# Kernel tuning notes

Hardware: AMD Instinct MI355X
Metric: run time of the kernel (lower is better)

## Reference

```python
import jax, jax.numpy as jnp
import numpy as np

HIDDEN = 1024
HEADS = 16
HEAD_DIM = HIDDEN // HEADS


def setup_inputs() -> dict:
    key = jax.random.key(0)
    ks = jax.random.split(key, 12)
    B, S, D = 2, 2048, HIDDEN
    scale = 1.0 / np.sqrt(D)
    return {
        "query": jax.random.normal(ks[0], (B, S, D), jnp.float32),
        "key": jax.random.normal(ks[1], (B, S, D), jnp.float32),
        "value": jax.random.normal(ks[2], (B, S, D), jnp.float32),
        "Wq": jax.random.normal(ks[3], (D, D), jnp.float32) * scale,
        "bq": jnp.zeros((D,), jnp.float32),
        "Wk": jax.random.normal(ks[4], (D, D), jnp.float32) * scale,
        "bk": jnp.zeros((D,), jnp.float32),
        "Wv": jax.random.normal(ks[5], (D, D), jnp.float32) * scale,
        "bv": jnp.zeros((D,), jnp.float32),
        "Wo": jax.random.normal(ks[6], (D, D), jnp.float32) * scale,
        "bo": jnp.zeros((D,), jnp.float32),
    }


def reference(query, key, value, Wq, bq, Wk, bk, Wv, bv, Wo, bo):
    B, S, D = query.shape
    H, Hd = HEADS, HEAD_DIM
    sm_scale = 1.0 / jnp.sqrt(jnp.asarray(Hd, query.dtype))

    def proj(x, W, b):  # nn.Linear: x @ W.T + b, then split heads -> [B,H,S,Hd]
        y = jnp.einsum("bsd,ed->bse", x, W) + b
        return y.reshape(B, S, H, Hd).transpose(0, 2, 1, 3)

    Q = proj(query, Wq, bq)
    K = proj(key, Wk, bk)
    V = proj(value, Wv, bv)

    scores = jnp.einsum("bhqd,bhkd->bhqk", Q, K) * sm_scale  # [B,H,S,S]
    attn = jax.nn.softmax(scores, axis=-1)
    ctx = jnp.einsum("bhqk,bhkd->bhqd", attn, V)
    ctx = ctx.transpose(0, 2, 1, 3).reshape(B, S, D)
    out = jnp.einsum("bsd,ed->bse", ctx, Wo) + bo
    return out
```

## Files before the change

kernel.cpp:

```cpp
#include <hip/hip_runtime.h>
#include <stdint.h>

typedef unsigned short u16;
typedef unsigned int u32;
typedef __attribute__((ext_vector_type(8))) short s16x8;
typedef __attribute__((ext_vector_type(4))) float fx4;

#define AS_GLOBAL __attribute__((address_space(1)))
#define AS_LDS    __attribute__((address_space(3)))

__device__ __forceinline__ void g2l16(const u16* g, u16* l) {
  __builtin_amdgcn_global_load_lds((const AS_GLOBAL unsigned int*)g,
                                   (AS_LDS unsigned int*)l, 16, 0, 0);
}
__device__ __forceinline__ u16 f2bf(float f) {
  u32 u = __float_as_uint(f);
  u += 0x7FFF + ((u >> 16) & 1);
  return (u16)(u >> 16);
}
__device__ __forceinline__ u32 pk2bf(float a, float b) {
  return (u32)f2bf(a) | ((u32)f2bf(b) << 16);
}

__global__ __launch_bounds__(256) void cvt3(const float* __restrict__ a, const float* __restrict__ b,
                                            const float* __restrict__ c, u16* oa, u16* ob, u16* oc, int n4) {
  const float* src = blockIdx.y == 0 ? a : blockIdx.y == 1 ? b : c;
  u16* dst = blockIdx.y == 0 ? oa : blockIdx.y == 1 ? ob : oc;
  int i = blockIdx.x * 256 + threadIdx.x;
  if (i >= n4) return;
  float4 f = ((const float4*)src)[i];
  ushort4 o; o.x = f2bf(f.x); o.y = f2bf(f.y); o.z = f2bf(f.z); o.w = f2bf(f.w);
  ((ushort4*)dst)[i] = o;
}
__global__ __launch_bounds__(256) void cvt4(const float* __restrict__ a, const float* __restrict__ b,
                                            const float* __restrict__ c, const float* __restrict__ d,
                                            u16* oa, u16* ob, u16* oc, u16* od, int n4) {
  const float* src = blockIdx.y == 0 ? a : blockIdx.y == 1 ? b : blockIdx.y == 2 ? c : d;
  u16* dst = blockIdx.y == 0 ? oa : blockIdx.y == 1 ? ob : blockIdx.y == 2 ? oc : od;
  int i = blockIdx.x * 256 + threadIdx.x;
  if (i >= n4) return;
  float4 f = ((const float4*)src)[i];
  ushort4 o; o.x = f2bf(f.x); o.y = f2bf(f.y); o.z = f2bf(f.z); o.w = f2bf(f.w);
  ((ushort4*)dst)[i] = o;
}

__global__ __launch_bounds__(256) void gemm_qkv(
    const u16* __restrict__ Aq, const u16* __restrict__ Ak, const u16* __restrict__ Av,
    const u16* __restrict__ Wq, const u16* __restrict__ Wk, const u16* __restrict__ Wv,
    const float* __restrict__ bq, const float* __restrict__ bk, const float* __restrict__ bv,
    u16* __restrict__ Oq, u16* __restrict__ Ok, u16* __restrict__ Ov)
{
  constexpr int K = 1024;
  __shared__ u16 As[128 * 32];
  __shared__ u16 Bs[128 * 32];
  const int z = blockIdx.z;
  const u16* A = z == 0 ? Aq : z == 1 ? Ak : Av;
  const u16* W = z == 0 ? Wq : z == 1 ? Wk : Wv;
  const float* bias = z == 0 ? bq : z == 1 ? bk : bv;
  u16* outB = z == 0 ? Oq : z == 1 ? Ok : Ov;
  const float scale = z == 0 ? 0.180336880f : 1.0f;

  const int bm = blockIdx.x, bn = blockIdx.y;
  const int tid = threadIdx.x;
  const int lane = tid & 63, wave = tid >> 6;
  const int quad = lane >> 4, col = lane & 15;
  const int wm = wave >> 1, wn = wave & 1;

  const int L0 = tid, L1 = 256 + tid;
  const int r0 = L0 >> 2, c0 = (L0 & 3) ^ ((r0 >> 1) & 3);
  const int r1 = L1 >> 2, c1 = (L1 & 3) ^ ((r1 >> 1) & 3);
  const u16* gA0 = A + (bm * 128 + r0) * K + c0 * 8;
  const u16* gA1 = A + (bm * 128 + r1) * K + c1 * 8;
  const u16* gB0 = W + (bn * 128 + r0) * K + c0 * 8;
  const u16* gB1 = W + (bn * 128 + r1) * K + c1 * 8;
  u16* lA0 = As + L0 * 8; u16* lA1 = As + L1 * 8;
  u16* lB0 = Bs + L0 * 8; u16* lB1 = Bs + L1 * 8;

  const int aRow = wm * 64 + col;
  const int bRow = wn * 64 + col;

  fx4 zero = {0.f, 0.f, 0.f, 0.f};
  fx4 acc[4][4];
#pragma unroll
  for (int i = 0; i < 4; ++i)
#pragma unroll
    for (int j = 0; j < 4; ++j) acc[i][j] = zero;

  for (int kb = 0; kb < K / 32; ++kb) {
    __syncthreads();
    g2l16(gA0 + kb * 32, lA0);
    g2l16(gA1 + kb * 32, lA1);
    g2l16(gB0 + kb * 32, lB0);
    g2l16(gB1 + kb * 32, lB1);
    __syncthreads();
    s16x8 af[4], bf[4];
#pragma unroll
    for (int mt = 0; mt < 4; ++mt) {
      int row = aRow + mt * 16;
      int ch = row * 4 + (quad ^ ((row >> 1) & 3));
      af[mt] = *(const s16x8*)(As + ch * 8);
    }
#pragma unroll
    for (int nt = 0; nt < 4; ++nt) {
      int row = bRow + nt * 16;
      int ch = row * 4 + (quad ^ ((row >> 1) & 3));
      bf[nt] = *(const s16x8*)(Bs + ch * 8);
    }
#pragma unroll
    for (int mt = 0; mt < 4; ++mt)
#pragma unroll
      for (int nt = 0; nt < 4; ++nt)
        acc[mt][nt] = __builtin_amdgcn_mfma_f32_16x16x32_bf16(af[mt], bf[nt], acc[mt][nt], 0, 0, 0);
  }

#pragma unroll
  for (int nt = 0; nt < 4; ++nt) {
    int n = bn * 128 + wn * 64 + nt * 16 + col;
    float bvv = bias[n];
#pragma unroll
    for (int mt = 0; mt < 4; ++mt) {
      int mbase = bm * 128 + wm * 64 + mt * 16 + quad * 4;
#pragma unroll
      for (int reg = 0; reg < 4; ++reg) {
        int m = mbase + reg;
        float v = (acc[mt][nt][reg] + bvv) * scale;
        int b = m >> 11, s = m & 2047;
        int h = n >> 6, hd = n & 63;
        outB[((b * 16 + h) * 2048 + s) * 64 + hd] = f2bf(v);
      }
    }
  }
}

__global__ __launch_bounds__(256) void gemm_out(
    const u16* __restrict__ A, const u16* __restrict__ W,
    const float* __restrict__ bias, float* __restrict__ outF)
{
  constexpr int K = 1024;
  __shared__ u16 As[128 * 32];
  __shared__ u16 Bs[64 * 32];
  const int bm = blockIdx.x, bn = blockIdx.y;
  const int tid = threadIdx.x;
  const int lane = tid & 63, wave = tid >> 6;
  const int quad = lane >> 4, col = lane & 15;
  const int wm = wave >> 1, wn = wave & 1;

  const int L0 = tid, L1 = 256 + tid;
  const int r0 = L0 >> 2, c0 = (L0 & 3) ^ ((r0 >> 1) & 3);
  const int r1 = L1 >> 2, c1 = (L1 & 3) ^ ((r1 >> 1) & 3);
  const u16* gA0 = A + (bm * 128 + r0) * K + c0 * 8;
  const u16* gA1 = A + (bm * 128 + r1) * K + c1 * 8;
  const u16* gB0 = W + (bn * 64 + r0) * K + c0 * 8;
  u16* lA0 = As + L0 * 8; u16* lA1 = As + L1 * 8;
  u16* lB0 = Bs + L0 * 8;

  const int aRow = wm * 64 + col;
  const int bRow = wn * 32 + col;

  fx4 zero = {0.f, 0.f, 0.f, 0.f};
  fx4 acc[4][2];
#pragma unroll
  for (int i = 0; i < 4; ++i)
#pragma unroll
    for (int j = 0; j < 2; ++j) acc[i][j] = zero;

  for (int kb = 0; kb < K / 32; ++kb) {
    __syncthreads();
    g2l16(gA0 + kb * 32, lA0);
    g2l16(gA1 + kb * 32, lA1);
    g2l16(gB0 + kb * 32, lB0);
    __syncthreads();
    s16x8 af[4], bf[2];
#pragma unroll
    for (int mt = 0; mt < 4; ++mt) {
      int row = aRow + mt * 16;
      int ch = row * 4 + (quad ^ ((row >> 1) & 3));
      af[mt] = *(const s16x8*)(As + ch * 8);
    }
#pragma unroll
    for (int nt = 0; nt < 2; ++nt) {
      int row = bRow + nt * 16;
      int ch = row * 4 + (quad ^ ((row >> 1) & 3));
      bf[nt] = *(const s16x8*)(Bs + ch * 8);
    }
#pragma unroll
    for (int mt = 0; mt < 4; ++mt)
#pragma unroll
      for (int nt = 0; nt < 2; ++nt)
        acc[mt][nt] = __builtin_amdgcn_mfma_f32_16x16x32_bf16(af[mt], bf[nt], acc[mt][nt], 0, 0, 0);
  }

#pragma unroll
  for (int nt = 0; nt < 2; ++nt) {
    int n = bn * 64 + wn * 32 + nt * 16 + col;
    float bvv = bias[n];
#pragma unroll
    for (int mt = 0; mt < 4; ++mt) {
      int mbase = bm * 128 + wm * 64 + mt * 16 + quad * 4;
#pragma unroll
      for (int reg = 0; reg < 4; ++reg)
        outF[(mbase + reg) * 1024 + n] = acc[mt][nt][reg] + bvv;
    }
  }
}

__global__ __launch_bounds__(256) void transpose_v(const u16* __restrict__ V,
                                                   u16* __restrict__ Vt) {
  __shared__ u16 tile[64 * 72];
  const int bh = blockIdx.y, s0 = blockIdx.x * 64;
  const int tid = threadIdx.x;
#pragma unroll
  for (int i = 0; i < 2; ++i) {
    int idx = i * 256 + tid;
    int s = idx >> 3, c = idx & 7;
    uint4 v = *(const uint4*)(V + ((size_t)bh * 2048 + s0 + s) * 64 + c * 8);
    const u16* pv = (const u16*)&v;
#pragma unroll
    for (int j = 0; j < 8; ++j) tile[(c * 8 + j) * 72 + s] = pv[j];
  }
  __syncthreads();
#pragma unroll
  for (int i = 0; i < 2; ++i) {
    int idx = i * 256 + tid;
    int d = idx >> 3, c = idx & 7;
    uint4 v = *(const uint4*)(tile + d * 72 + c * 8);
    *(uint4*)(Vt + ((size_t)bh * 64 + d) * 2048 + s0 + c * 8) = v;
  }
}

__global__ __launch_bounds__(256, 4) void flash_attn(
    const u16* __restrict__ Qp, const u16* __restrict__ Kp,
    const u16* __restrict__ Vt, u16* __restrict__ ctx)
{
  __shared__ u16 sh[16384];
  const int qt = blockIdx.x, bh = blockIdx.y;
  const int tid = threadIdx.x, lane = tid & 63, wave = tid >> 6;
  const int quad = lane >> 4, col = lane & 15;
  const int wm = wave >> 1, wn = wave & 1;

  const u16* Qb = Qp + ((size_t)bh * 2048 + qt * 64) * 64;
  const u16* Kb = Kp + (size_t)bh * 2048 * 64;
  const u16* Vb = Vt + (size_t)bh * 64 * 2048;

  s16x8 qf[2][2];
#pragma unroll
  for (int mt = 0; mt < 2; ++mt)
#pragma unroll
    for (int h = 0; h < 2; ++h)
      qf[mt][h] = *(const s16x8*)(Qb + (wm * 32 + mt * 16 + col) * 64 + h * 32 + quad * 8);

  fx4 zero = {0.f, 0.f, 0.f, 0.f};
  fx4 acc_o[2][4], acc_l[2];
#pragma unroll
  for (int mt = 0; mt < 2; ++mt) {
    acc_l[mt] = zero;
#pragma unroll
    for (int dt = 0; dt < 4; ++dt) acc_o[mt][dt] = zero;
  }
  s16x8 ones;
#pragma unroll
  for (int j = 0; j < 8; ++j) ones[j] = (short)0x3F80;

  u16* Vs = sh;
  u16* Pw = sh + 8192 + wave * 2048;

  for (int kv = 0; kv < 16; ++kv) {
    const int n0 = kv * 128;
    __syncthreads();
#pragma unroll
    for (int i = 0; i < 4; ++i) {
      int idx = wave * 256 + i * 64 + lane;
      int d = idx >> 4, c = idx & 15;
      uint4 v = *(const uint4*)(Vb + d * 2048 + n0 + c * 8);
      *(uint4*)(Vs + d * 128 + (c ^ (d & 15)) * 8) = v;
    }
#pragma unroll
    for (int nt = 0; nt < 4; ++nt) {
      const u16* kr = Kb + (n0 + wn * 64 + nt * 16 + col) * 64 + quad * 8;
      s16x8 k0 = *(const s16x8*)(kr);
      s16x8 k1 = *(const s16x8*)(kr + 32);
#pragma unroll
      for (int mt = 0; mt < 2; ++mt) {
        fx4 s = __builtin_amdgcn_mfma_f32_16x16x32_bf16(k0, qf[mt][0], zero, 0, 0, 0);
        s = __builtin_amdgcn_mfma_f32_16x16x32_bf16(k1, qf[mt][1], s, 0, 0, 0);
        int m = mt * 16 + col;
        int cch = 2 * nt + (quad >> 1);
        uint2 w;
        w.x = pk2bf(exp2f(s[0]), exp2f(s[1]));
        w.y = pk2bf(exp2f(s[2]), exp2f(s[3]));
        *(uint2*)(Pw + m * 64 + ((cch ^ (m & 7))) * 8 + (quad & 1) * 4) = w;
      }
    }
    __syncthreads();
#pragma unroll
    for (int ks = 0; ks < 2; ++ks) {
      s16x8 pf[2];
#pragma unroll
      for (int mt = 0; mt < 2; ++mt)
        pf[mt] = *(const s16x8*)(Pw + (mt * 16 + col) * 64 + ((4 * ks + quad) ^ (col & 7)) * 8);
#pragma unroll
      for (int dt = 0; dt < 4; ++dt) {
        s16x8 vf = *(const s16x8*)(Vs + (dt * 16 + col) * 128 + ((wn * 8 + 4 * ks + quad) ^ col) * 8);
#pragma unroll
        for (int mt = 0; mt < 2; ++mt)
          acc_o[mt][dt] = __builtin_amdgcn_mfma_f32_16x16x32_bf16(pf[mt], vf, acc_o[mt][dt], 0, 0, 0);
      }
#pragma unroll
      for (int mt = 0; mt < 2; ++mt)
        acc_l[mt] = __builtin_amdgcn_mfma_f32_16x16x32_bf16(pf[mt], ones, acc_l[mt], 0, 0, 0);
    }
  }

  __syncthreads();
  float* buf = (float*)sh;
  if (wn == 1) {
#pragma unroll
    for (int mt = 0; mt < 2; ++mt) {
#pragma unroll
      for (int dt = 0; dt < 4; ++dt)
#pragma unroll
        for (int e = 0; e < 4; ++e)
          buf[wm * 2560 + ((mt * 4 + dt) * 4 + e) * 64 + lane] = acc_o[mt][dt][e];
#pragma unroll
      for (int e = 0; e < 4; ++e)
        buf[wm * 2560 + (32 + mt * 4 + e) * 64 + lane] = acc_l[mt][e];
    }
  }
  __syncthreads();
  if (wn == 0) {
    const int b = bh >> 4, h = bh & 15;
#pragma unroll
    for (int mt = 0; mt < 2; ++mt) {
      fx4 rl;
#pragma unroll
      for (int e = 0; e < 4; ++e) {
        float l = acc_l[mt][e] + buf[wm * 2560 + (32 + mt * 4 + e) * 64 + lane];
        rl[e] = 1.0f / l;
      }
#pragma unroll
      for (int dt = 0; dt < 4; ++dt)
#pragma unroll
        for (int e = 0; e < 4; ++e) {
          float v = (acc_o[mt][dt][e] + buf[wm * 2560 + ((mt * 4 + dt) * 4 + e) * 64 + lane]) * rl[e];
          int s = qt * 64 + wm * 32 + mt * 16 + quad * 4 + e;
          ctx[((size_t)(b * 2048 + s)) * 1024 + h * 64 + dt * 16 + col] = f2bf(v);
        }
    }
  }
}

extern "C" void kernel_launch(void* const* d_in, const int* in_sizes, int n_in,
                              void* d_out, int out_size, void* d_ws, size_t ws_size,
                              hipStream_t stream) {
  const float* q  = (const float*)d_in[0];
  const float* k  = (const float*)d_in[1];
  const float* v  = (const float*)d_in[2];
  const float* Wq = (const float*)d_in[3];
  const float* bq = (const float*)d_in[4];
  const float* Wk = (const float*)d_in[5];
  const float* bk = (const float*)d_in[6];
  const float* Wv = (const float*)d_in[7];
  const float* bv = (const float*)d_in[8];
  const float* Wo = (const float*)d_in[9];
  const float* bo = (const float*)d_in[10];
  float* out = (float*)d_out;

  char* ws = (char*)d_ws;
  const size_t MB = 1u << 20;
  u16* qb  = (u16*)(ws + 0 * MB);
  u16* kb  = (u16*)(ws + 8 * MB);
  u16* vb  = (u16*)(ws + 16 * MB);
  u16* wqb = (u16*)(ws + 24 * MB);
  u16* wkb = (u16*)(ws + 26 * MB);
  u16* wvb = (u16*)(ws + 28 * MB);
  u16* wob = (u16*)(ws + 30 * MB);
  u16* Qp  = (u16*)(ws + 32 * MB);
  u16* Kp  = (u16*)(ws + 40 * MB);
  u16* Vp  = (u16*)(ws + 48 * MB);
  u16* Vtp = (u16*)(ws + 56 * MB);
  u16* ctx = (u16*)(ws + 64 * MB);

  cvt3<<<dim3(4096, 3), 256, 0, stream>>>(q, k, v, qb, kb, vb, 1048576);
  cvt4<<<dim3(1024, 4), 256, 0, stream>>>(Wq, Wk, Wv, Wo, wqb, wkb, wvb, wob, 262144);

  gemm_qkv<<<dim3(32, 8, 3), 256, 0, stream>>>(qb, kb, vb, wqb, wkb, wvb,
                                               bq, bk, bv, Qp, Kp, Vp);
  transpose_v<<<dim3(32, 32), 256, 0, stream>>>(Vp, Vtp);
  flash_attn<<<dim3(32, 32), 256, 0, stream>>>(Qp, Kp, Vtp, ctx);
  gemm_out<<<dim3(32, 16), 256, 0, stream>>>(ctx, wob, bo, out);
}
```

Baseline: 259.7 us.

## Fuse V transpose into QKV epilogue and keep P in registers for attention

The QKV GEMM epilogue now writes V directly in transposed [bh, d, s] layout, which removes the separate transpose kernel and its round trip through global memory. The flash-attention kernel no longer stages V and P through LDS. The probabilities stay in registers and feed 16x16x16 MFMAs, with V fragments loaded straight from global memory, which drops the two per-iteration block syncs. The two conversion kernels are merged into one launch. The tradeoffs are uncached, narrower V loads from global memory in the inner loop, twice as many MFMA instructions at half depth, and a removed occupancy hint.

```diff
diff --git a/kernel.cpp b/kernel.cpp
--- a/kernel.cpp
+++ b/kernel.cpp
@@ -4,6 +4,7 @@
 typedef unsigned short u16;
 typedef unsigned int u32;
 typedef __attribute__((ext_vector_type(8))) short s16x8;
+typedef __attribute__((ext_vector_type(4))) short s16x4;
 typedef __attribute__((ext_vector_type(4))) float fx4;
 
 #define AS_GLOBAL __attribute__((address_space(1)))
@@ -22,33 +23,34 @@
   return (u32)f2bf(a) | ((u32)f2bf(b) << 16);
 }
 
-__global__ __launch_bounds__(256) void cvt3(const float* __restrict__ a, const float* __restrict__ b,
-                                            const float* __restrict__ c, u16* oa, u16* ob, u16* oc, int n4) {
-  const float* src = blockIdx.y == 0 ? a : blockIdx.y == 1 ? b : c;
-  u16* dst = blockIdx.y == 0 ? oa : blockIdx.y == 1 ? ob : oc;
+__global__ __launch_bounds__(256) void cvt_all(
+    const float* __restrict__ q, const float* __restrict__ k, const float* __restrict__ v,
+    const float* __restrict__ wq, const float* __restrict__ wk, const float* __restrict__ wv,
+    const float* __restrict__ wo,
+    u16* oq, u16* ok, u16* ov, u16* owq, u16* owk, u16* owv, u16* owo) {
+  const int y = blockIdx.y;
+  const float* src; u16* dst; int n4;
+  switch (y) {
+    case 0: src = q;  dst = oq;  n4 = 1048576; break;
+    case 1: src = k;  dst = ok;  n4 = 1048576; break;
+    case 2: src = v;  dst = ov;  n4 = 1048576; break;
+    case 3: src = wq; dst = owq; n4 = 262144; break;
+    case 4: src = wk; dst = owk; n4 = 262144; break;
+    case 5: src = wv; dst = owv; n4 = 262144; break;
+    default: src = wo; dst = owo; n4 = 262144; break;
+  }
   int i = blockIdx.x * 256 + threadIdx.x;
   if (i >= n4) return;
   float4 f = ((const float4*)src)[i];
   ushort4 o; o.x = f2bf(f.x); o.y = f2bf(f.y); o.z = f2bf(f.z); o.w = f2bf(f.w);
   ((ushort4*)dst)[i] = o;
 }
-__global__ __launch_bounds__(256) void cvt4(const float* __restrict__ a, const float* __restrict__ b,
-                                            const float* __restrict__ c, const float* __restrict__ d,
-                                            u16* oa, u16* ob, u16* oc, u16* od, int n4) {
-  const float* src = blockIdx.y == 0 ? a : blockIdx.y == 1 ? b : blockIdx.y == 2 ? c : d;
-  u16* dst = blockIdx.y == 0 ? oa : blockIdx.y == 1 ? ob : blockIdx.y == 2 ? oc : od;
-  int i = blockIdx.x * 256 + threadIdx.x;
-  if (i >= n4) return;
-  float4 f = ((const float4*)src)[i];
-  ushort4 o; o.x = f2bf(f.x); o.y = f2bf(f.y); o.z = f2bf(f.z); o.w = f2bf(f.w);
-  ((ushort4*)dst)[i] = o;
-}
 
 __global__ __launch_bounds__(256) void gemm_qkv(
     const u16* __restrict__ Aq, const u16* __restrict__ Ak, const u16* __restrict__ Av,
     const u16* __restrict__ Wq, const u16* __restrict__ Wk, const u16* __restrict__ Wv,
     const float* __restrict__ bq, const float* __restrict__ bk, const float* __restrict__ bv,
-    u16* __restrict__ Oq, u16* __restrict__ Ok, u16* __restrict__ Ov)
+    u16* __restrict__ Oq, u16* __restrict__ Ok, u16* __restrict__ OvT)
 {
   constexpr int K = 1024;
   __shared__ u16 As[128 * 32];
@@ -57,7 +59,6 @@
   const u16* A = z == 0 ? Aq : z == 1 ? Ak : Av;
   const u16* W = z == 0 ? Wq : z == 1 ? Wk : Wv;
   const float* bias = z == 0 ? bq : z == 1 ? bk : bv;
-  u16* outB = z == 0 ? Oq : z == 1 ? Ok : Ov;
   const float scale = z == 0 ? 0.180336880f : 1.0f;
 
   const int bm = blockIdx.x, bn = blockIdx.y;
@@ -116,17 +117,22 @@
 #pragma unroll
   for (int nt = 0; nt < 4; ++nt) {
     int n = bn * 128 + wn * 64 + nt * 16 + col;
+    int h = n >> 6, hd = n & 63;
     float bvv = bias[n];
 #pragma unroll
     for (int mt = 0; mt < 4; ++mt) {
       int mbase = bm * 128 + wm * 64 + mt * 16 + quad * 4;
-#pragma unroll
-      for (int reg = 0; reg < 4; ++reg) {
-        int m = mbase + reg;
-        float v = (acc[mt][nt][reg] + bvv) * scale;
-        int b = m >> 11, s = m & 2047;
-        int h = n >> 6, hd = n & 63;
-        outB[((b * 16 + h) * 2048 + s) * 64 + hd] = f2bf(v);
+      int b = mbase >> 11, s = mbase & 2047;
+      if (z == 2) {
+        uint2 w;
+        w.x = pk2bf(acc[mt][nt][0] + bvv, acc[mt][nt][1] + bvv);
+        w.y = pk2bf(acc[mt][nt][2] + bvv, acc[mt][nt][3] + bvv);
+        *(uint2*)(OvT + (((size_t)(b * 16 + h) * 64 + hd) * 2048 + s)) = w;
+      } else {
+        u16* dst = (z == 0 ? Oq : Ok) + ((size_t)(b * 16 + h) * 2048 + s) * 64 + hd;
+#pragma unroll
+        for (int reg = 0; reg < 4; ++reg)
+          dst[(size_t)reg * 64] = f2bf((acc[mt][nt][reg] + bvv) * scale);
       }
     }
   }
@@ -204,35 +210,11 @@
   }
 }
 
-__global__ __launch_bounds__(256) void transpose_v(const u16* __restrict__ V,
-                                                   u16* __restrict__ Vt) {
-  __shared__ u16 tile[64 * 72];
-  const int bh = blockIdx.y, s0 = blockIdx.x * 64;
-  const int tid = threadIdx.x;
-#pragma unroll
-  for (int i = 0; i < 2; ++i) {
-    int idx = i * 256 + tid;
-    int s = idx >> 3, c = idx & 7;
-    uint4 v = *(const uint4*)(V + ((size_t)bh * 2048 + s0 + s) * 64 + c * 8);
-    const u16* pv = (const u16*)&v;
-#pragma unroll
-    for (int j = 0; j < 8; ++j) tile[(c * 8 + j) * 72 + s] = pv[j];
-  }
-  __syncthreads();
-#pragma unroll
-  for (int i = 0; i < 2; ++i) {
-    int idx = i * 256 + tid;
-    int d = idx >> 3, c = idx & 7;
-    uint4 v = *(const uint4*)(tile + d * 72 + c * 8);
-    *(uint4*)(Vt + ((size_t)bh * 64 + d) * 2048 + s0 + c * 8) = v;
-  }
-}
-
-__global__ __launch_bounds__(256, 4) void flash_attn(
+__global__ __launch_bounds__(256) void flash_attn(
     const u16* __restrict__ Qp, const u16* __restrict__ Kp,
     const u16* __restrict__ Vt, u16* __restrict__ ctx)
 {
-  __shared__ u16 sh[16384];
+  __shared__ float buf[5120];
   const int qt = blockIdx.x, bh = blockIdx.y;
   const int tid = threadIdx.x, lane = tid & 63, wave = tid >> 6;
   const int quad = lane >> 4, col = lane & 15;
@@ -257,62 +239,44 @@
 #pragma unroll
     for (int dt = 0; dt < 4; ++dt) acc_o[mt][dt] = zero;
   }
-  s16x8 ones;
-#pragma unroll
-  for (int j = 0; j < 8; ++j) ones[j] = (short)0x3F80;
-
-  u16* Vs = sh;
-  u16* Pw = sh + 8192 + wave * 2048;
+  s16x4 ones;
+#pragma unroll
+  for (int j = 0; j < 4; ++j) ones[j] = (short)0x3F80;
 
   for (int kv = 0; kv < 16; ++kv) {
-    const int n0 = kv * 128;
-    __syncthreads();
-#pragma unroll
-    for (int i = 0; i < 4; ++i) {
-      int idx = wave * 256 + i * 64 + lane;
-      int d = idx >> 4, c = idx & 15;
-      uint4 v = *(const uint4*)(Vb + d * 2048 + n0 + c * 8);
-      *(uint4*)(Vs + d * 128 + (c ^ (d & 15)) * 8) = v;
-    }
+    const int n0 = kv * 128 + wn * 64;
+    s16x4 pf[4][2];
 #pragma unroll
     for (int nt = 0; nt < 4; ++nt) {
-      const u16* kr = Kb + (n0 + wn * 64 + nt * 16 + col) * 64 + quad * 8;
+      const u16* kr = Kb + (n0 + nt * 16 + col) * 64 + quad * 8;
       s16x8 k0 = *(const s16x8*)(kr);
       s16x8 k1 = *(const s16x8*)(kr + 32);
 #pragma unroll
       for (int mt = 0; mt < 2; ++mt) {
         fx4 s = __builtin_amdgcn_mfma_f32_16x16x32_bf16(k0, qf[mt][0], zero, 0, 0, 0);
         s = __builtin_amdgcn_mfma_f32_16x16x32_bf16(k1, qf[mt][1], s, 0, 0, 0);
-        int m = mt * 16 + col;
-        int cch = 2 * nt + (quad >> 1);
-        uint2 w;
-        w.x = pk2bf(exp2f(s[0]), exp2f(s[1]));
-        w.y = pk2bf(exp2f(s[2]), exp2f(s[3]));
-        *(uint2*)(Pw + m * 64 + ((cch ^ (m & 7))) * 8 + (quad & 1) * 4) = w;
+        union { uint2 d; s16x4 v; } u;
+        u.d.x = pk2bf(exp2f(s[0]), exp2f(s[1]));
+        u.d.y = pk2bf(exp2f(s[2]), exp2f(s[3]));
+        pf[nt][mt] = u.v;
       }
     }
-    __syncthreads();
-#pragma unroll
-    for (int ks = 0; ks < 2; ++ks) {
-      s16x8 pf[2];
+#pragma unroll
+    for (int nt = 0; nt < 4; ++nt) {
 #pragma unroll
       for (int mt = 0; mt < 2; ++mt)
-        pf[mt] = *(const s16x8*)(Pw + (mt * 16 + col) * 64 + ((4 * ks + quad) ^ (col & 7)) * 8);
+        acc_l[mt] = __builtin_amdgcn_mfma_f32_16x16x16bf16_1k(pf[nt][mt], ones, acc_l[mt], 0, 0, 0);
 #pragma unroll
       for (int dt = 0; dt < 4; ++dt) {
-        s16x8 vf = *(const s16x8*)(Vs + (dt * 16 + col) * 128 + ((wn * 8 + 4 * ks + quad) ^ col) * 8);
+        s16x4 vf = *(const s16x4*)(Vb + (dt * 16 + col) * 2048 + n0 + nt * 16 + quad * 4);
 #pragma unroll
         for (int mt = 0; mt < 2; ++mt)
-          acc_o[mt][dt] = __builtin_amdgcn_mfma_f32_16x16x32_bf16(pf[mt], vf, acc_o[mt][dt], 0, 0, 0);
+          acc_o[mt][dt] = __builtin_amdgcn_mfma_f32_16x16x16bf16_1k(pf[nt][mt], vf, acc_o[mt][dt], 0, 0, 0);
       }
-#pragma unroll
-      for (int mt = 0; mt < 2; ++mt)
-        acc_l[mt] = __builtin_amdgcn_mfma_f32_16x16x32_bf16(pf[mt], ones, acc_l[mt], 0, 0, 0);
     }
   }
 
   __syncthreads();
-  float* buf = (float*)sh;
   if (wn == 1) {
 #pragma unroll
     for (int mt = 0; mt < 2; ++mt) {
@@ -376,16 +340,13 @@
   u16* wob = (u16*)(ws + 30 * MB);
   u16* Qp  = (u16*)(ws + 32 * MB);
   u16* Kp  = (u16*)(ws + 40 * MB);
-  u16* Vp  = (u16*)(ws + 48 * MB);
-  u16* Vtp = (u16*)(ws + 56 * MB);
-  u16* ctx = (u16*)(ws + 64 * MB);
-
-  cvt3<<<dim3(4096, 3), 256, 0, stream>>>(q, k, v, qb, kb, vb, 1048576);
-  cvt4<<<dim3(1024, 4), 256, 0, stream>>>(Wq, Wk, Wv, Wo, wqb, wkb, wvb, wob, 262144);
-
+  u16* Vtp = (u16*)(ws + 48 * MB);
+  u16* ctx = (u16*)(ws + 56 * MB);
+
+  cvt_all<<<dim3(4096, 7), 256, 0, stream>>>(q, k, v, Wq, Wk, Wv, Wo,
+                                             qb, kb, vb, wqb, wkb, wvb, wob);
   gemm_qkv<<<dim3(32, 8, 3), 256, 0, stream>>>(qb, kb, vb, wqb, wkb, wvb,
-                                               bq, bk, bv, Qp, Kp, Vp);
-  transpose_v<<<dim3(32, 32), 256, 0, stream>>>(Vp, Vtp);
+                                               bq, bk, bv, Qp, Kp, Vtp);
   flash_attn<<<dim3(32, 32), 256, 0, stream>>>(Qp, Kp, Vtp, ctx);
   gemm_out<<<dim3(32, 16), 256, 0, stream>>>(ctx, wob, bo, out);
 }
```

New measurement: 398.1 us. 53.3% more time.
